# Kernel optimization log

Measured on AMD Instinct MI355X. Metric: run time of the kernel, lower is better.

The kernel has to match this reference:

```python
import jax, jax.numpy as jnp
import numpy as np

NUM_FEAT = 10

def _flatten(x):
    # [B,T,C,H,W] -> [B,C,T*H*W]
    B, T, C, H, W = x.shape
    return jnp.transpose(x, (0, 2, 1, 3, 4)).reshape(B, C, T * H * W)

def _conv1x1(w, b, x):
    # pointwise Conv1d: w [F,C], b [F], x [B,C,N] -> [B,F,N]
    return jnp.einsum('fc,bcn->bfn', w, x) + b[None, :, None]

def setup_inputs() -> dict:
    key = jax.random.key(0)
    ks = jax.random.split(key, 9)
    B, T, C, H, W = 1, 5, 64, 32, 32
    F = NUM_FEAT
    return {
        'input1': jax.random.normal(ks[0], (B, T, C, H, W), jnp.float32),
        'input2': jax.random.normal(ks[1], (B, T, C, H, W), jnp.float32),
        'act_weights': jax.random.uniform(ks[2], (3,), jnp.float32),
        'conv1_w': jax.random.normal(ks[3], (F, C), jnp.float32) * 0.05,
        'conv1_b': jnp.zeros((F,), jnp.float32),
        'conv2_w': jax.random.normal(ks[4], (F, C), jnp.float32) * 0.05,
        'conv2_b': jnp.zeros((F,), jnp.float32),
        'g3_w': jax.random.normal(ks[5], (F, C), jnp.float32) * 0.05,
        'g3_b': jnp.zeros((F,), jnp.float32),
    }

def reference(input1, input2, act_weights, conv1_w, conv1_b, conv2_w, conv2_b, g3_w, g3_b):
    B, T, C, H, W = input1.shape
    F = conv1_w.shape[0]
    x1 = _flatten(input1)                    # [B,C,N]
    x2 = _flatten(input2)                    # [B,C,N]
    q = _conv1x1(conv1_w, conv1_b, x1)       # [B,F,N]
    k = _conv1x1(conv2_w, conv2_b, x2)       # [B,F,N]
    v = _conv1x1(g3_w, g3_b, x1)             # [B,F,N]
    scores = jnp.einsum('bfn,bfm->bnm', q, k)  # [B,N,N] (same math, computed once)

    def branch(act_scores):
        o = jnp.einsum('bnm,bfm->bnf', act_scores, v)      # [B,N,F]
        o = o.reshape(B, T, H, W, F)
        return jnp.transpose(o, (0, 1, 4, 2, 3))           # [B,T,F,H,W]

    out = act_weights[0] * branch(jax.nn.relu(scores))
    out = out + act_weights[1] * branch(jax.nn.sigmoid(scores))
    # NOTE: original code scales the softmax branch by act_weights[0] (bug kept faithfully)
    out = out + act_weights[0] * branch(jax.nn.softmax(scores, axis=1))
    return out
```

## Files before the change

### kernel.cpp

```cpp
#include <hip/hip_runtime.h>

#define N_TOK   5120
#define C_IN    64
#define F_OUT   10
#define FP      12

#define DTILE   40
#define MTILE   40

__global__ __launch_bounds__(256) void qkv_kernel(
    const float* __restrict__ x1, const float* __restrict__ x2,
    const float* __restrict__ w1, const float* __restrict__ b1,
    const float* __restrict__ w2, const float* __restrict__ b2,
    const float* __restrict__ w3, const float* __restrict__ b3,
    float* __restrict__ Q, float* __restrict__ K, float* __restrict__ V)
{
    int arr = blockIdx.x / 200;
    int rem = blockIdx.x - arr * 200;
    int f   = rem / 20;
    int nbk = rem - f * 20;
    int n   = nbk * 256 + threadIdx.x;
    int t = n >> 10, p = n & 1023;

    const float* x    = (arr == 1) ? x2 : x1;
    const float* w    = (arr == 0) ? w1 : (arr == 1) ? w2 : w3;
    const float* bias = (arr == 0) ? b1 : (arr == 1) ? b2 : b3;
    float*       dst  = (arr == 0) ? Q  : (arr == 1) ? K  : V;

    const float* xp = x + t * (C_IN * 1024) + p;
    const float* wr = w + f * C_IN;

    float4 wv[16];
#pragma unroll
    for (int i = 0; i < 16; ++i) wv[i] = ((const float4*)wr)[i];

    float acc = 0.f;
#pragma unroll
    for (int i = 0; i < 16; ++i) {
        acc = fmaf(wv[i].x, xp[(4 * i + 0) * 1024], acc);
        acc = fmaf(wv[i].y, xp[(4 * i + 1) * 1024], acc);
        acc = fmaf(wv[i].z, xp[(4 * i + 2) * 1024], acc);
        acc = fmaf(wv[i].w, xp[(4 * i + 3) * 1024], acc);
    }
    dst[n * FP + f] = acc + bias[f];
}

__global__ __launch_bounds__(256) void denom_kernel(
    const float* __restrict__ Q, const float* __restrict__ K,
    float* __restrict__ dpart, int nclen)
{
    int mTile = blockIdx.x % 5;
    int nc    = blockIdx.x / 5;
    int tid   = threadIdx.x;
    int m0 = mTile * 1024 + tid;

    float kk[4][10];
#pragma unroll
    for (int c = 0; c < 4; ++c) {
        const float* kp = K + (m0 + c * 256) * FP;
        float4 a = ((const float4*)kp)[0];
        float4 b = ((const float4*)kp)[1];
        float2 e = ((const float2*)kp)[4];
        kk[c][0]=a.x; kk[c][1]=a.y; kk[c][2]=a.z; kk[c][3]=a.w;
        kk[c][4]=b.x; kk[c][5]=b.y; kk[c][6]=b.z; kk[c][7]=b.w;
        kk[c][8]=e.x; kk[c][9]=e.y;
    }

    __shared__ __align__(16) float sq[DTILE * FP];

    float d[4] = {0.f, 0.f, 0.f, 0.f};
    int n0 = nc * nclen;
    for (int base = n0; base < n0 + nclen; base += DTILE) {
        __syncthreads();
        if (tid < DTILE * FP / 4)
            ((float4*)sq)[tid] = ((const float4*)(Q + base * FP))[tid];
        __syncthreads();
#pragma unroll 2
        for (int j = 0; j < DTILE; ++j) {
            const float4* qp = (const float4*)(sq + j * FP);
            float4 qa = qp[0], qb = qp[1], qc = qp[2];
            float qq[10] = {qa.x, qa.y, qa.z, qa.w, qb.x, qb.y, qb.z, qb.w,
                            qc.x, qc.y};
#pragma unroll
            for (int c = 0; c < 4; ++c) {
                float s = 0.f;
#pragma unroll
                for (int f = 0; f < F_OUT; ++f) s = fmaf(qq[f], kk[c][f], s);
                d[c] += __expf(fminf(s, 60.f));
            }
        }
    }
#pragma unroll
    for (int c = 0; c < 4; ++c) dpart[nc * N_TOK + m0 + c * 256] = d[c];
}

__global__ __launch_bounds__(256) void invw_kernel(
    const float* __restrict__ dpart, const float* __restrict__ aw,
    float* __restrict__ K, int nchunks)
{
    int m = blockIdx.x * 256 + threadIdx.x;
    float d = 0.f;
#pragma unroll 8
    for (int c = 0; c < nchunks; ++c) d += dpart[c * N_TOK + m];
    K[m * FP + 10] = aw[0] / d;
}

__global__ __launch_bounds__(256) void main_kernel(
    const float* __restrict__ Q, const float* __restrict__ K,
    const float* __restrict__ V, const float* __restrict__ aw,
    float* __restrict__ opart, int mclen)
{
    int nTile = blockIdx.x % 4;
    int mc    = blockIdx.x / 4;
    int tid   = threadIdx.x;
    int nb = nTile * 1280 + tid;
    float w0 = aw[0], w1v = aw[1];

    float q[5][10];
#pragma unroll
    for (int r = 0; r < 5; ++r) {
        const float* qp = Q + (nb + r * 256) * FP;
        float4 a = ((const float4*)qp)[0];
        float4 b = ((const float4*)qp)[1];
        float2 e = ((const float2*)qp)[4];
        q[r][0]=a.x; q[r][1]=a.y; q[r][2]=a.z; q[r][3]=a.w;
        q[r][4]=b.x; q[r][5]=b.y; q[r][6]=b.z; q[r][7]=b.w;
        q[r][8]=e.x; q[r][9]=e.y;
    }

    float acc[5][F_OUT];
#pragma unroll
    for (int r = 0; r < 5; ++r)
#pragma unroll
        for (int f = 0; f < F_OUT; ++f) acc[r][f] = 0.f;

    __shared__ __align__(16) float sk[MTILE * FP];
    __shared__ __align__(16) float sv[MTILE * FP];

    int mstart = mc * mclen;
    for (int mbase = mstart; mbase < mstart + mclen; mbase += MTILE) {
        __syncthreads();
        if (tid < 120)
            ((float4*)sk)[tid] = ((const float4*)(K + mbase * FP))[tid];
        else if (tid < 240)
            ((float4*)sv)[tid - 120] = ((const float4*)(V + mbase * FP))[tid - 120];
        __syncthreads();

#pragma unroll 2
        for (int j = 0; j < MTILE; ++j) {
            const float4* kp = (const float4*)(sk + j * FP);
            float4 ka = kp[0], kb = kp[1], kc = kp[2];
            float kk[10] = {ka.x, ka.y, ka.z, ka.w, kb.x, kb.y, kb.z, kb.w,
                            kc.x, kc.y};
            float iw = kc.z;
            const float4* vp = (const float4*)(sv + j * FP);
            float4 va = vp[0], vb = vp[1], vc = vp[2];
            float vv[10] = {va.x, va.y, va.z, va.w, vb.x, vb.y, vb.z, vb.w,
                            vc.x, vc.y};

#pragma unroll
            for (int r = 0; r < 5; ++r) {
                float s = 0.f;
#pragma unroll
                for (int f = 0; f < F_OUT; ++f) s = fmaf(q[r][f], kk[f], s);
                float rl = fmaxf(s, 0.f);
                float e  = __expf(fminf(s, 60.f));
                float sg = e * __builtin_amdgcn_rcpf(1.f + e);
                float cf = fmaf(e, iw, fmaf(w1v, sg, w0 * rl));
#pragma unroll
                for (int f = 0; f < F_OUT; ++f) acc[r][f] = fmaf(cf, vv[f], acc[r][f]);
            }
        }
    }

#pragma unroll
    for (int r = 0; r < 5; ++r) {
        float2* o = (float2*)(opart + (size_t)(mc * N_TOK + nb + r * 256) * F_OUT);
#pragma unroll
        for (int f = 0; f < 5; ++f)
            o[f] = make_float2(acc[r][2 * f], acc[r][2 * f + 1]);
    }
}

__global__ __launch_bounds__(256) void reduce_kernel(
    const float* __restrict__ opart, float* __restrict__ out, int mchunks)
{
    int idx = blockIdx.x * 256 + threadIdx.x;
    float s = 0.f;
#pragma unroll 16
    for (int c = 0; c < mchunks; ++c) s += opart[c * (N_TOK * F_OUT) + idx];
    unsigned un = (unsigned)idx / 10u;
    int n = (int)un;
    int f = idx - n * 10;
    int t = n >> 10, p = n & 1023;
    out[((t * F_OUT + f) << 10) + p] = s;
}

extern "C" void kernel_launch(void* const* d_in, const int* in_sizes, int n_in,
                              void* d_out, int out_size, void* d_ws, size_t ws_size,
                              hipStream_t stream)
{
    const float* in1 = (const float*)d_in[0];
    const float* in2 = (const float*)d_in[1];
    const float* aw  = (const float*)d_in[2];
    const float* w1  = (const float*)d_in[3];
    const float* b1  = (const float*)d_in[4];
    const float* w2  = (const float*)d_in[5];
    const float* b2  = (const float*)d_in[6];
    const float* w3  = (const float*)d_in[7];
    const float* b3  = (const float*)d_in[8];
    float* out = (float*)d_out;

    int nchunks, mchunks;
    if (ws_size >= (size_t)32 << 20) { nchunks = 128; mchunks = 128; }
    else                             { nchunks = 32;  mchunks = 32;  }
    int nclen = N_TOK / nchunks;
    int mclen = N_TOK / mchunks;

    float* ws    = (float*)d_ws;
    float* Q     = ws;
    float* K     = Q + N_TOK * FP;
    float* V     = K + N_TOK * FP;
    float* dpart = V + N_TOK * FP;
    float* opart = dpart + nchunks * N_TOK;

    qkv_kernel<<<600, 256, 0, stream>>>(in1, in2, w1, b1, w2, b2, w3, b3, Q, K, V);
    denom_kernel<<<5 * nchunks, 256, 0, stream>>>(Q, K, dpart, nclen);
    invw_kernel<<<N_TOK / 256, 256, 0, stream>>>(dpart, aw, K, nchunks);
    main_kernel<<<4 * mchunks, 256, 0, stream>>>(Q, K, V, aw, opart, mclen);
    reduce_kernel<<<(N_TOK * F_OUT) / 256, 256, 0, stream>>>(opart, out, mchunks);
}
```

Measured before the change: 137.0 us.

## Fold inverse-denominator pass into main kernel and retune chunking and occupancy

Removes the separate invw kernel: each main_kernel block now sums the denominator partials for its own m-chunk into shared memory, which saves a launch and a write back into K. Tile sizes and chunk counts become template constants. Rows per thread drop from 5 to 4, with 5 n-tiles per chunk, and launch_bounds now ask for 4 waves per SIMD to raise occupancy. The qkv kernel loads weights inside the loop instead of preloading them. The risks are that each main block redundantly re-reads dpart, and there is less Q reuse per K/V tile.

New measurement: 139.9 us. 1.02x slower.

```diff
diff --git a/kernel.cpp b/kernel.cpp
--- a/kernel.cpp
+++ b/kernel.cpp
@@ -4,9 +4,8 @@
 #define C_IN    64
 #define F_OUT   10
 #define FP      12
-
-#define DTILE   40
-#define MTILE   40
+#define DTILE   20
+#define MTILE   20
 
 __global__ __launch_bounds__(256) void qkv_kernel(
     const float* __restrict__ x1, const float* __restrict__ x2,
@@ -30,25 +29,24 @@
     const float* xp = x + t * (C_IN * 1024) + p;
     const float* wr = w + f * C_IN;
 
-    float4 wv[16];
-#pragma unroll
-    for (int i = 0; i < 16; ++i) wv[i] = ((const float4*)wr)[i];
-
     float acc = 0.f;
 #pragma unroll
     for (int i = 0; i < 16; ++i) {
-        acc = fmaf(wv[i].x, xp[(4 * i + 0) * 1024], acc);
-        acc = fmaf(wv[i].y, xp[(4 * i + 1) * 1024], acc);
-        acc = fmaf(wv[i].z, xp[(4 * i + 2) * 1024], acc);
-        acc = fmaf(wv[i].w, xp[(4 * i + 3) * 1024], acc);
+        float4 wv = ((const float4*)wr)[i];
+        acc = fmaf(wv.x, xp[(4 * i + 0) * 1024], acc);
+        acc = fmaf(wv.y, xp[(4 * i + 1) * 1024], acc);
+        acc = fmaf(wv.z, xp[(4 * i + 2) * 1024], acc);
+        acc = fmaf(wv.w, xp[(4 * i + 3) * 1024], acc);
     }
     dst[n * FP + f] = acc + bias[f];
 }
 
-__global__ __launch_bounds__(256) void denom_kernel(
+template<int NCH>
+__global__ __launch_bounds__(256, 4) void denom_kernel(
     const float* __restrict__ Q, const float* __restrict__ K,
-    float* __restrict__ dpart, int nclen)
-{
+    float* __restrict__ dpart)
+{
+    const int nclen = N_TOK / NCH;
     int mTile = blockIdx.x % 5;
     int nc    = blockIdx.x / 5;
     int tid   = threadIdx.x;
@@ -94,31 +92,34 @@
     for (int c = 0; c < 4; ++c) dpart[nc * N_TOK + m0 + c * 256] = d[c];
 }
 
-__global__ __launch_bounds__(256) void invw_kernel(
-    const float* __restrict__ dpart, const float* __restrict__ aw,
-    float* __restrict__ K, int nchunks)
-{
-    int m = blockIdx.x * 256 + threadIdx.x;
-    float d = 0.f;
+template<int NCH, int MCH>
+__global__ __launch_bounds__(256, 4) void main_kernel(
+    const float* __restrict__ Q, const float* __restrict__ K,
+    const float* __restrict__ V, const float* __restrict__ dpart,
+    const float* __restrict__ aw, float* __restrict__ opart)
+{
+    const int mclen = N_TOK / MCH;
+    int nTile = blockIdx.x % 5;
+    int mc    = blockIdx.x / 5;
+    int tid   = threadIdx.x;
+    int nb = nTile * 1024 + tid;
+    int mstart = mc * mclen;
+    float w0 = aw[0], w1v = aw[1];
+
+    __shared__ __align__(16) float sk[MTILE * FP];
+    __shared__ __align__(16) float sv[MTILE * FP];
+    __shared__ float siw[320];
+
+    for (int t = tid; t < mclen; t += 256) {
+        float d = 0.f;
 #pragma unroll 8
-    for (int c = 0; c < nchunks; ++c) d += dpart[c * N_TOK + m];
-    K[m * FP + 10] = aw[0] / d;
-}
-
-__global__ __launch_bounds__(256) void main_kernel(
-    const float* __restrict__ Q, const float* __restrict__ K,
-    const float* __restrict__ V, const float* __restrict__ aw,
-    float* __restrict__ opart, int mclen)
-{
-    int nTile = blockIdx.x % 4;
-    int mc    = blockIdx.x / 4;
-    int tid   = threadIdx.x;
-    int nb = nTile * 1280 + tid;
-    float w0 = aw[0], w1v = aw[1];
-
-    float q[5][10];
-#pragma unroll
-    for (int r = 0; r < 5; ++r) {
+        for (int c = 0; c < NCH; ++c) d += dpart[c * N_TOK + mstart + t];
+        siw[t] = w0 / d;
+    }
+
+    float q[4][10];
+#pragma unroll
+    for (int r = 0; r < 4; ++r) {
         const float* qp = Q + (nb + r * 256) * FP;
         float4 a = ((const float4*)qp)[0];
         float4 b = ((const float4*)qp)[1];
@@ -128,22 +129,18 @@
         q[r][8]=e.x; q[r][9]=e.y;
     }
 
-    float acc[5][F_OUT];
-#pragma unroll
-    for (int r = 0; r < 5; ++r)
+    float acc[4][F_OUT];
+#pragma unroll
+    for (int r = 0; r < 4; ++r)
 #pragma unroll
         for (int f = 0; f < F_OUT; ++f) acc[r][f] = 0.f;
 
-    __shared__ __align__(16) float sk[MTILE * FP];
-    __shared__ __align__(16) float sv[MTILE * FP];
-
-    int mstart = mc * mclen;
     for (int mbase = mstart; mbase < mstart + mclen; mbase += MTILE) {
         __syncthreads();
-        if (tid < 120)
+        if (tid < 60)
             ((float4*)sk)[tid] = ((const float4*)(K + mbase * FP))[tid];
-        else if (tid < 240)
-            ((float4*)sv)[tid - 120] = ((const float4*)(V + mbase * FP))[tid - 120];
+        else if (tid < 120)
+            ((float4*)sv)[tid - 60] = ((const float4*)(V + mbase * FP))[tid - 60];
         __syncthreads();
 
 #pragma unroll 2
@@ -152,14 +149,14 @@
             float4 ka = kp[0], kb = kp[1], kc = kp[2];
             float kk[10] = {ka.x, ka.y, ka.z, ka.w, kb.x, kb.y, kb.z, kb.w,
                             kc.x, kc.y};
-            float iw = kc.z;
             const float4* vp = (const float4*)(sv + j * FP);
             float4 va = vp[0], vb = vp[1], vc = vp[2];
             float vv[10] = {va.x, va.y, va.z, va.w, vb.x, vb.y, vb.z, vb.w,
                             vc.x, vc.y};
-
-#pragma unroll
-            for (int r = 0; r < 5; ++r) {
+            float iw = siw[mbase - mstart + j];
+
+#pragma unroll
+            for (int r = 0; r < 4; ++r) {
                 float s = 0.f;
 #pragma unroll
                 for (int f = 0; f < F_OUT; ++f) s = fmaf(q[r][f], kk[f], s);
@@ -168,13 +165,14 @@
                 float sg = e * __builtin_amdgcn_rcpf(1.f + e);
                 float cf = fmaf(e, iw, fmaf(w1v, sg, w0 * rl));
 #pragma unroll
-                for (int f = 0; f < F_OUT; ++f) acc[r][f] = fmaf(cf, vv[f], acc[r][f]);
+                for (int f = 0; f < F_OUT; ++f)
+                    acc[r][f] = fmaf(cf, vv[f], acc[r][f]);
             }
         }
     }
 
 #pragma unroll
-    for (int r = 0; r < 5; ++r) {
+    for (int r = 0; r < 4; ++r) {
         float2* o = (float2*)(opart + (size_t)(mc * N_TOK + nb + r * 256) * F_OUT);
 #pragma unroll
         for (int f = 0; f < 5; ++f)
@@ -182,18 +180,38 @@
     }
 }
 
+template<int MCH>
 __global__ __launch_bounds__(256) void reduce_kernel(
-    const float* __restrict__ opart, float* __restrict__ out, int mchunks)
+    const float* __restrict__ opart, float* __restrict__ out)
 {
     int idx = blockIdx.x * 256 + threadIdx.x;
     float s = 0.f;
 #pragma unroll 16
-    for (int c = 0; c < mchunks; ++c) s += opart[c * (N_TOK * F_OUT) + idx];
+    for (int c = 0; c < MCH; ++c) s += opart[c * (N_TOK * F_OUT) + idx];
     unsigned un = (unsigned)idx / 10u;
     int n = (int)un;
     int f = idx - n * 10;
     int t = n >> 10, p = n & 1023;
     out[((t * F_OUT + f) << 10) + p] = s;
+}
+
+template<int NCH, int MCH>
+static void run_all(const float* in1, const float* in2, const float* aw,
+                    const float* w1, const float* b1,
+                    const float* w2, const float* b2,
+                    const float* w3, const float* b3,
+                    float* out, float* ws, hipStream_t stream)
+{
+    float* Q     = ws;
+    float* K     = Q + N_TOK * FP;
+    float* V     = K + N_TOK * FP;
+    float* dpart = V + N_TOK * FP;
+    float* opart = dpart + NCH * N_TOK;
+
+    qkv_kernel<<<600, 256, 0, stream>>>(in1, in2, w1, b1, w2, b2, w3, b3, Q, K, V);
+    denom_kernel<NCH><<<5 * NCH, 256, 0, stream>>>(Q, K, dpart);
+    main_kernel<NCH, MCH><<<5 * MCH, 256, 0, stream>>>(Q, K, V, dpart, aw, opart);
+    reduce_kernel<MCH><<<(N_TOK * F_OUT) / 256, 256, 0, stream>>>(opart, out);
 }
 
 extern "C" void kernel_launch(void* const* d_in, const int* in_sizes, int n_in,
@@ -210,23 +228,12 @@
     const float* w3  = (const float*)d_in[7];
     const float* b3  = (const float*)d_in[8];
     float* out = (float*)d_out;
-
-    int nchunks, mchunks;
-    if (ws_size >= (size_t)32 << 20) { nchunks = 128; mchunks = 128; }
-    else                             { nchunks = 32;  mchunks = 32;  }
-    int nclen = N_TOK / nchunks;
-    int mclen = N_TOK / mchunks;
-
-    float* ws    = (float*)d_ws;
-    float* Q     = ws;
-    float* K     = Q + N_TOK * FP;
-    float* V     = K + N_TOK * FP;
-    float* dpart = V + N_TOK * FP;
-    float* opart = dpart + nchunks * N_TOK;
-
-    qkv_kernel<<<600, 256, 0, stream>>>(in1, in2, w1, b1, w2, b2, w3, b3, Q, K, V);
-    denom_kernel<<<5 * nchunks, 256, 0, stream>>>(Q, K, dpart, nclen);
-    invw_kernel<<<N_TOK / 256, 256, 0, stream>>>(dpart, aw, K, nchunks);
-    main_kernel<<<4 * mchunks, 256, 0, stream>>>(Q, K, V, aw, opart, mclen);
-    reduce_kernel<<<(N_TOK * F_OUT) / 256, 256, 0, stream>>>(opart, out, mchunks);
-}
+    float* ws  = (float*)d_ws;
+
+    if (ws_size >= ((size_t)48 << 20))
+        run_all<256, 128>(in1, in2, aw, w1, b1, w2, b2, w3, b3, out, ws, stream);
+    else if (ws_size >= ((size_t)16 << 20))
+        run_all<64, 64>(in1, in2, aw, w1, b1, w2, b2, w3, b3, out, ws, stream);
+    else
+        run_all<16, 16>(in1, in2, aw, w1, b1, w2, b2, w3, b3, out, ws, stream);
+}
```
